# Kernel tuning notes

Measured on AMD Instinct MI355X. Metric: run time of the kernel, lower is better.

The kernel has to match this reference:

```python
import jax, jax.numpy as jnp
import numpy as np

N_NODES = 100000
IN_CH = 2
HID = 64
K = 3
N_EDGES = 1600000


def _cheb_norm(edge_index, num_nodes):
    # PyG ChebConv sym normalization with lambda_max=2.0:
    # L_hat = L - I = -D^{-1/2} A D^{-1/2} (zero diagonal, edge_weight=1)
    src, dst = edge_index[0], edge_index[1]
    deg = jax.ops.segment_sum(jnp.ones(src.shape[0], jnp.float32), src,
                              num_segments=num_nodes)
    dinv = jnp.where(deg > 0, jax.lax.rsqrt(jnp.maximum(deg, 1.0)), 0.0)
    norm = -dinv[src] * dinv[dst]  # [E]
    return src, dst, norm


def _cheb_conv(x, src, dst, norm, W, b, num_nodes):
    # W: [K, in, out], b: [out]
    def prop(t):  # sparse L_hat @ t via gather/scatter
        return jax.ops.segment_sum(norm[:, None] * t[src], dst,
                                   num_segments=num_nodes)
    Tx0 = x
    out = Tx0 @ W[0]
    Tx1 = prop(Tx0)
    out = out + Tx1 @ W[1]
    for k in range(2, W.shape[0]):
        Tx2 = 2.0 * prop(Tx1) - Tx0
        out = out + Tx2 @ W[k]
        Tx0, Tx1 = Tx1, Tx2
    return out + b


def setup_inputs() -> dict:
    key = jax.random.key(0)
    ks = jax.random.split(key, 16)
    x = jax.random.normal(ks[0], (N_NODES, IN_CH), jnp.float32)
    edge_index = jax.random.randint(ks[1], (2, N_EDGES), 0, N_NODES,
                                    dtype=jnp.int64)
    h = jax.random.normal(ks[2], (N_NODES, HID), jnp.float32)
    s1 = 1.0 / np.sqrt(IN_CH)
    s2 = 1.0 / np.sqrt(HID)
    sg = 1.0 / np.sqrt(2 * HID)
    W1 = jax.random.uniform(ks[3], (K, IN_CH, HID), jnp.float32, -s1, s1)
    b1 = jnp.zeros((HID,), jnp.float32)
    W2 = jax.random.uniform(ks[4], (K, HID, HID), jnp.float32, -s2, s2)
    b2 = jnp.zeros((HID,), jnp.float32)
    Wz = jax.random.uniform(ks[5], (2 * HID, HID), jnp.float32, -sg, sg)
    bz = jax.random.uniform(ks[6], (HID,), jnp.float32, -sg, sg)
    Wr = jax.random.uniform(ks[7], (2 * HID, HID), jnp.float32, -sg, sg)
    br = jax.random.uniform(ks[8], (HID,), jnp.float32, -sg, sg)
    Wc = jax.random.uniform(ks[9], (2 * HID, HID), jnp.float32, -sg, sg)
    bc = jax.random.uniform(ks[10], (HID,), jnp.float32, -sg, sg)
    return {"x": x, "edge_index": edge_index, "h": h,
            "W1": W1, "b1": b1, "W2": W2, "b2": b2,
            "Wz": Wz, "bz": bz, "Wr": Wr, "br": br, "Wc": Wc, "bc": bc}


def reference(x, edge_index, h, W1, b1, W2, b2, Wz, bz, Wr, br, Wc, bc):
    num_nodes = x.shape[0]
    src, dst, norm = _cheb_norm(edge_index, num_nodes)
    input_conv = _cheb_conv(x, src, dst, norm, W1, b1, num_nodes)
    hidden_conv = _cheb_conv(h, src, dst, norm, W2, b2, num_nodes)
    combined = jnp.concatenate([input_conv, hidden_conv], axis=1)
    z = jax.nn.sigmoid(combined @ Wz + bz)
    r = jax.nn.sigmoid(combined @ Wr + br)
    comb_c = jnp.concatenate([input_conv, r * hidden_conv], axis=1)
    h_tilde = jnp.tanh(comb_c @ Wc + bc)
    return z * h + (1.0 - z) * h_tilde
```

## Files before the change

### kernel.cpp

```cpp
#include <hip/hip_runtime.h>
#include <hip/hip_bf16.h>
#include <math.h>

#define HID 64
#define NBA 512
#define NBUCK 256
#define BSHIFT 9
#define BINS 512
#define NBN (NBUCK * NBA)

typedef __attribute__((ext_vector_type(8))) short bf16x8;
typedef __attribute__((ext_vector_type(4))) float f32x4;

__device__ __forceinline__ unsigned int bf16r(float f) {
    unsigned int u = __float_as_uint(f);
    return (u + 0x7fffu + ((u >> 16) & 1u)) >> 16;
}
__device__ __forceinline__ unsigned int pack2(float a, float b) {
    return bf16r(a) | (bf16r(b) << 16);
}
__device__ __forceinline__ float lo2f(unsigned int u) { return __uint_as_float(u << 16); }
__device__ __forceinline__ float hi2f(unsigned int u) { return __uint_as_float(u & 0xffff0000u); }

__device__ __forceinline__ bf16x8 asbf(uint4 u) {
    union { uint4 u4; bf16x8 b; } c; c.u4 = u; return c.b;
}
__device__ __forceinline__ void load8(const float* p, float* d) {
    float4 a = *(const float4*)p, b = *(const float4*)(p + 4);
    d[0]=a.x; d[1]=a.y; d[2]=a.z; d[3]=a.w; d[4]=b.x; d[5]=b.y; d[6]=b.z; d[7]=b.w;
}

__global__ void bucketA_kernel(const int* __restrict__ ei, int E,
                               int* __restrict__ cntsc) {
    __shared__ int cd[NBUCK], cs[NBUCK];
    int t = threadIdx.x;
    cd[t] = 0; cs[t] = 0;
    __syncthreads();
    int ce = (E + NBA - 1) / NBA;
    int e0 = blockIdx.x * ce, e1 = min(e0 + ce, E);
    for (int e = e0 + t; e < e1; e += 256) {
        int s = ei[e], d = ei[E + e];
        atomicAdd(&cs[s >> BSHIFT], 1);
        atomicAdd(&cd[d >> BSHIFT], 1);
    }
    __syncthreads();
    cntsc[t * NBA + blockIdx.x]       = cd[t];
    cntsc[NBN + t * NBA + blockIdx.x] = cs[t];
}

__global__ void scanA_kernel(const int* __restrict__ cnt, int* __restrict__ bs, int N) {
    __shared__ int s[256];
    int t = threadIdx.x, n = blockIdx.x * 256 + t;
    s[t] = (n < N) ? cnt[n] : 0;
    __syncthreads();
    for (int off = 128; off > 0; off >>= 1) {
        if (t < off) s[t] += s[t + off];
        __syncthreads();
    }
    if (t == 0) bs[blockIdx.x] = s[0];
}

__global__ void scanB_kernel(int* __restrict__ bs, int nb) {
    __shared__ int s[1024];
    int t = threadIdx.x;
    int orig = (t < nb) ? bs[t] : 0;
    s[t] = orig;
    __syncthreads();
    for (int off = 1; off < 1024; off <<= 1) {
        int v = (t >= off) ? s[t - off] : 0;
        __syncthreads();
        s[t] += v;
        __syncthreads();
    }
    if (t < nb) bs[t] = s[t] - orig;
}

__global__ void scanC_kernel(const int* __restrict__ cnt, const int* __restrict__ bs,
                             int* __restrict__ outp, int N) {
    __shared__ int s[256];
    int t = threadIdx.x, n = blockIdx.x * 256 + t;
    int c = (n < N) ? cnt[n] : 0;
    s[t] = c;
    __syncthreads();
    for (int off = 1; off < 256; off <<= 1) {
        int v = (t >= off) ? s[t - off] : 0;
        __syncthreads();
        s[t] += v;
        __syncthreads();
    }
    if (n < N) outp[n] = bs[blockIdx.x] + s[t] - c;
}

__global__ void bucketB_kernel(const int* __restrict__ ei, int E,
                               const int* __restrict__ scanned,
                               unsigned int* __restrict__ dstrec,
                               int* __restrict__ srckeys) {
    __shared__ int cd[NBUCK], cs[NBUCK], bd[NBUCK], bsr[NBUCK];
    int t = threadIdx.x;
    cd[t] = 0; cs[t] = 0;
    bd[t]  = scanned[t * NBA + blockIdx.x];
    bsr[t] = scanned[NBN + t * NBA + blockIdx.x] - E;
    __syncthreads();
    int ce = (E + NBA - 1) / NBA;
    int e0 = blockIdx.x * ce, e1 = min(e0 + ce, E);
    for (int e = e0 + t; e < e1; e += 256) {
        int s = ei[e], d = ei[E + e];
        int db = d >> BSHIFT, sb = s >> BSHIFT;
        int rd = atomicAdd(&cd[db], 1);
        dstrec[bd[db] + rd] = (unsigned int)s | ((unsigned int)(d & (BINS - 1)) << 17);
        int rs = atomicAdd(&cs[sb], 1);
        srckeys[bsr[sb] + rs] = s;
    }
}

__global__ void bucketC2_kernel(const int* __restrict__ srckeys,
                                const int* __restrict__ scanned,
                                float* __restrict__ dinv, int N, int E) {
    __shared__ int deg[BINS];
    int b = blockIdx.x, t = threadIdx.x;
    deg[t] = 0;
    __syncthreads();
    int start = scanned[NBN + b * NBA] - E;
    int end   = (b < NBUCK - 1) ? scanned[NBN + (b + 1) * NBA] - E : E;
    for (int i = start + t; i < end; i += BINS)
        atomicAdd(&deg[srckeys[i] & (BINS - 1)], 1);
    __syncthreads();
    int node = (b << BSHIFT) + t;
    if (node < N) {
        int dg = deg[t];
        dinv[node] = dg > 0 ? rsqrtf((float)dg) : 0.0f;
    }
}

__global__ void bucketC1_kernel(const unsigned int* __restrict__ dstrec,
                                const int* __restrict__ scanned,
                                const float* __restrict__ dinv,
                                int* __restrict__ row, int* __restrict__ cnt,
                                int2* __restrict__ srcw, int N, int E) {
    __shared__ int lc[BINS], ls[BINS], lr[BINS];
    int b = blockIdx.x, t = threadIdx.x;
    lc[t] = 0; lr[t] = 0;
    __syncthreads();
    int start = scanned[b * NBA];
    int end   = (b < NBUCK - 1) ? scanned[(b + 1) * NBA] : E;
    for (int i = start + t; i < end; i += BINS)
        atomicAdd(&lc[dstrec[i] >> 17], 1);
    __syncthreads();
    ls[t] = lc[t];
    __syncthreads();
    for (int off = 1; off < BINS; off <<= 1) {
        int v = (t >= off) ? ls[t - off] : 0;
        __syncthreads();
        ls[t] += v;
        __syncthreads();
    }
    int rl = start + ls[t] - lc[t];
    int node = (b << BSHIFT) + t;
    if (node < N) { row[node] = rl; cnt[node] = lc[t]; }
    __syncthreads();
    ls[t] = rl;
    __syncthreads();
    for (int i = start + t; i < end; i += BINS) {
        unsigned int rec = dstrec[i];
        int bin = (int)(rec >> 17);
        int src = (int)(rec & 0x1FFFFu);
        int p = ls[bin] + atomicAdd(&lr[bin], 1);
        srcw[p] = make_int2(src, __float_as_int(dinv[src]));
    }
}

__global__ void packwT_kernel(const float* __restrict__ W2, const float* __restrict__ Wz,
                              const float* __restrict__ Wr, const float* __restrict__ Wc,
                              unsigned int* __restrict__ WT) {
    int idx = blockIdx.x * blockDim.x + threadIdx.x;
    if (idx >= 18432) return;
    float v0, v1;
    if (idx < 6144) {
        int c = idx / 96, kk = idx % 96;
        int k0 = 2 * kk;
        if (k0 < 64) {
            v0 = W2[k0 * 64 + c] - W2[8192 + k0 * 64 + c];
            v1 = W2[(k0 + 1) * 64 + c] - W2[8192 + (k0 + 1) * 64 + c];
        } else if (k0 < 128) {
            v0 = W2[4096 + (k0 - 64) * 64 + c];
            v1 = W2[4096 + (k0 - 63) * 64 + c];
        } else {
            v0 = 2.0f * W2[8192 + (k0 - 128) * 64 + c];
            v1 = 2.0f * W2[8192 + (k0 - 127) * 64 + c];
        }
    } else if (idx < 14336) {
        int t = idx - 6144;
        int c = t / 64, kk = t % 64, k0 = 2 * kk;
        const float* Ws = (c < 64) ? Wz : Wr;
        int cc = c & 63;
        v0 = Ws[k0 * 64 + cc];
        v1 = Ws[(k0 + 1) * 64 + cc];
    } else {
        int t = idx - 14336;
        int c = t / 64, kk = t % 64, k0 = 2 * kk;
        v0 = Wc[k0 * 64 + c];
        v1 = Wc[(k0 + 1) * 64 + c];
    }
    WT[idx] = pack2(v0, v1);
}

__global__ void packh_kernel(const float* __restrict__ h, unsigned int* __restrict__ hbf,
                             int total2) {
    int i = blockIdx.x * blockDim.x + threadIdx.x;
    if (i < total2) {
        float2 v = ((const float2*)h)[i];
        hbf[i] = pack2(v.x, v.y);
    }
}

#define FMA8(ww, vv, xvv) \
    a0 = fmaf(ww, lo2f(vv.x), a0); a1 = fmaf(ww, hi2f(vv.x), a1); \
    a2 = fmaf(ww, lo2f(vv.y), a2); a3 = fmaf(ww, hi2f(vv.y), a3); \
    a4 = fmaf(ww, lo2f(vv.z), a4); a5 = fmaf(ww, hi2f(vv.z), a5); \
    a6 = fmaf(ww, lo2f(vv.w), a6); a7 = fmaf(ww, hi2f(vv.w), a7); \
    ax0 = fmaf(ww, xvv.x, ax0);    ax1 = fmaf(ww, xvv.y, ax1);

__global__ void gather64_kernel(const int* __restrict__ row, const int* __restrict__ cnt,
                                const int2* __restrict__ srcw, const float* __restrict__ dinv,
                                const unsigned int* __restrict__ src,
                                const float2* __restrict__ xsrc,
                                unsigned int* __restrict__ dst,
                                float2* __restrict__ xdst, int N) {
    int wu = __builtin_amdgcn_readfirstlane((int)threadIdx.x >> 6);
    int n = blockIdx.x * 4 + wu;
    if (n >= N) return;
    int lane = threadIdx.x & 63;
    int t    = lane & 7;
    int slot = lane >> 3;
    int start = row[n], k = cnt[n];
    float a0 = 0, a1 = 0, a2 = 0, a3 = 0, a4 = 0, a5 = 0, a6 = 0, a7 = 0;
    float ax0 = 0, ax1 = 0;
    if (k <= 16) {
        if (slot < k) {
            int2 rec0 = srcw[start + slot];
            bool h1 = slot + 8 < k;
            int2 rec1 = h1 ? srcw[start + slot + 8] : rec0;
            uint4 v0 = ((const uint4*)(src + (size_t)rec0.x * 32))[t];
            uint4 v1 = ((const uint4*)(src + (size_t)rec1.x * 32))[t];
            float2 xv0 = xsrc[rec0.x];
            float2 xv1 = xsrc[rec1.x];
            float w0 = __int_as_float(rec0.y);
            float w1 = h1 ? __int_as_float(rec1.y) : 0.0f;
            FMA8(w0, v0, xv0)
            FMA8(w1, v1, xv1)
        }
    } else {
        for (int e = slot; e < k; e += 32) {
            int2 rec0 = srcw[start + e];
            bool h1 = (e + 8) < k, h2 = (e + 16) < k, h3 = (e + 24) < k;
            int2 rec1 = h1 ? srcw[start + e + 8]  : rec0;
            int2 rec2 = h2 ? srcw[start + e + 16] : rec0;
            int2 rec3 = h3 ? srcw[start + e + 24] : rec0;
            uint4 v0 = ((const uint4*)(src + (size_t)rec0.x * 32))[t];
            uint4 v1 = ((const uint4*)(src + (size_t)rec1.x * 32))[t];
            uint4 v2 = ((const uint4*)(src + (size_t)rec2.x * 32))[t];
            uint4 v3 = ((const uint4*)(src + (size_t)rec3.x * 32))[t];
            float2 xv0 = xsrc[rec0.x];
            float2 xv1 = xsrc[rec1.x];
            float2 xv2 = xsrc[rec2.x];
            float2 xv3 = xsrc[rec3.x];
            float w0 = __int_as_float(rec0.y);
            float w1 = h1 ? __int_as_float(rec1.y) : 0.0f;
            float w2 = h2 ? __int_as_float(rec2.y) : 0.0f;
            float w3 = h3 ? __int_as_float(rec3.y) : 0.0f;
            FMA8(w0, v0, xv0)
            FMA8(w1, v1, xv1)
            FMA8(w2, v2, xv2)
            FMA8(w3, v3, xv3)
        }
    }
    a0 += __shfl_xor(a0, 8);  a1 += __shfl_xor(a1, 8);
    a2 += __shfl_xor(a2, 8);  a3 += __shfl_xor(a3, 8);
    a4 += __shfl_xor(a4, 8);  a5 += __shfl_xor(a5, 8);
    a6 += __shfl_xor(a6, 8);  a7 += __shfl_xor(a7, 8);
    ax0 += __shfl_xor(ax0, 8);  ax1 += __shfl_xor(ax1, 8);
    a0 += __shfl_xor(a0, 16); a1 += __shfl_xor(a1, 16);
    a2 += __shfl_xor(a2, 16); a3 += __shfl_xor(a3, 16);
    a4 += __shfl_xor(a4, 16); a5 += __shfl_xor(a5, 16);
    a6 += __shfl_xor(a6, 16); a7 += __shfl_xor(a7, 16);
    ax0 += __shfl_xor(ax0, 16); ax1 += __shfl_xor(ax1, 16);
    a0 += __shfl_xor(a0, 32); a1 += __shfl_xor(a1, 32);
    a2 += __shfl_xor(a2, 32); a3 += __shfl_xor(a3, 32);
    a4 += __shfl_xor(a4, 32); a5 += __shfl_xor(a5, 32);
    a6 += __shfl_xor(a6, 32); a7 += __shfl_xor(a7, 32);
    ax0 += __shfl_xor(ax0, 32); ax1 += __shfl_xor(ax1, 32);
    if (slot == 0) {
        float dn = -dinv[n];
        unsigned int* drow = dst + (size_t)n * 32;
        uint4 o;
        o.x = pack2(dn * a0, dn * a1);
        o.y = pack2(dn * a2, dn * a3);
        o.z = pack2(dn * a4, dn * a5);
        o.w = pack2(dn * a6, dn * a7);
        ((uint4*)drow)[t] = o;
        if (t == 0)
            xdst[n] = make_float2(dn * ax0, dn * ax1);
    }
}

__global__ __launch_bounds__(256, 2) void gate_mfma_kernel(
    float* __restrict__ out,
    const float* __restrict__ x,
    const float* __restrict__ h,
    const float* __restrict__ txa,
    const float* __restrict__ txb,
    const unsigned int* __restrict__ t1u,
    const unsigned int* __restrict__ ppu,
    const float* __restrict__ W1, const float* __restrict__ b1,
    const unsigned int* __restrict__ WT,
    const float* __restrict__ b2, const float* __restrict__ bz,
    const float* __restrict__ br, const float* __restrict__ bc,
    int N) {
    __shared__ __align__(16) unsigned int s_wzr[128 * 68];
    __shared__ __align__(16) unsigned int s_wc [64 * 68];
    __shared__ unsigned short tr[4][32][72];

    int tid  = threadIdx.x;
    int lane = tid & 63;
    int wu   = __builtin_amdgcn_readfirstlane(tid >> 6);
    int q    = lane >> 4;
    int r16  = lane & 15;
    int base = blockIdx.x * 128 + wu * 32;

    int nA[2];
    nA[0] = min(base + r16, N - 1);
    nA[1] = min(base + 16 + r16, N - 1);

    const unsigned int* W2eT = WT;

    {
        const uint4* wzr4 = (const uint4*)(WT + 6144);
        const uint4* wc4  = (const uint4*)(WT + 14336);
        #pragma unroll
        for (int i = 0; i < 8; ++i) {
            int idx4 = tid + i * 256;
            uint4 v = wzr4[idx4];
            int r = idx4 >> 4, c4 = (idx4 & 15) * 4;
            *(uint4*)&s_wzr[r * 68 + c4] = v;
        }
        #pragma unroll
        for (int i = 0; i < 4; ++i) {
            int idx4 = tid + i * 256;
            uint4 v = wc4[idx4];
            int r = idx4 >> 4, c4 = (idx4 & 15) * 4;
            *(uint4*)&s_wc[r * 68 + c4] = v;
        }
    }

    uint4 icA[2][2];
    {
        float2 xv[2], tav[2], tbv[2];
        #pragma unroll
        for (int mt = 0; mt < 2; ++mt) {
            xv[mt]  = ((const float2*)x)[nA[mt]];
            tav[mt] = ((const float2*)txa)[nA[mt]];
            tbv[mt] = ((const float2*)txb)[nA[mt]];
        }
        #pragma unroll
        for (int kf = 0; kf < 2; ++kf) {
            int ch0 = kf * 32 + 8 * q;
            float b1s[8], w0[8], w1s[8], w2[8], w3[8], w4[8], w5[8];
            load8(b1 + ch0, b1s);
            load8(W1 + ch0, w0);       load8(W1 + 64 + ch0, w1s);
            load8(W1 + 128 + ch0, w2); load8(W1 + 192 + ch0, w3);
            load8(W1 + 256 + ch0, w4); load8(W1 + 320 + ch0, w5);
            #pragma unroll
            for (int mt = 0; mt < 2; ++mt) {
                float t20 = 2.0f * tbv[mt].x - xv[mt].x;
                float t21 = 2.0f * tbv[mt].y - xv[mt].y;
                unsigned int pr[4];
                #pragma unroll
                for (int p = 0; p < 4; ++p) {
                    float v0 = b1s[2*p]   + xv[mt].x * w0[2*p]   + xv[mt].y * w1s[2*p]
                             + tav[mt].x * w2[2*p]   + tav[mt].y * w3[2*p]
                             + t20 * w4[2*p]   + t21 * w5[2*p];
                    float v1 = b1s[2*p+1] + xv[mt].x * w0[2*p+1] + xv[mt].y * w1s[2*p+1]
                             + tav[mt].x * w2[2*p+1] + tav[mt].y * w3[2*p+1]
                             + t20 * w4[2*p+1] + t21 * w5[2*p+1];
                    pr[p] = pack2(v0, v1);
                }
                icA[mt][kf] = make_uint4(pr[0], pr[1], pr[2], pr[3]);
            }
        }
    }

    f32x4 acc1[2][4];
    #pragma unroll
    for (int mt = 0; mt < 2; ++mt)
        #pragma unroll
        for (int nt = 0; nt < 4; ++nt)
            acc1[mt][nt] = (f32x4){0.0f, 0.0f, 0.0f, 0.0f};

    #pragma unroll
    for (int ks = 0; ks < 6; ++ks) {
        bf16x8 a[2];
        if (ks < 2) {
            #pragma unroll
            for (int mt = 0; mt < 2; ++mt) {
                float hs[8];
                load8(h + (size_t)nA[mt] * 64 + ks * 32 + 8 * q, hs);
                uint4 u;
                u.x = pack2(hs[0], hs[1]); u.y = pack2(hs[2], hs[3]);
                u.z = pack2(hs[4], hs[5]); u.w = pack2(hs[6], hs[7]);
                a[mt] = asbf(u);
            }
        } else {
            const unsigned int* tab = (ks < 4) ? t1u : ppu;
            int ksl = ks & 1;
            #pragma unroll
            for (int mt = 0; mt < 2; ++mt)
                a[mt] = asbf(*(const uint4*)(tab + (size_t)nA[mt] * 32 + ksl * 16 + q * 4));
        }
        #pragma unroll
        for (int nt = 0; nt < 4; ++nt) {
            bf16x8 b = asbf(*(const uint4*)(W2eT + (nt * 16 + r16) * 96 + ks * 16 + q * 4));
            #pragma unroll
            for (int mt = 0; mt < 2; ++mt)
                acc1[mt][nt] = __builtin_amdgcn_mfma_f32_16x16x32_bf16(a[mt], b, acc1[mt][nt], 0, 0, 0);
        }
    }

    __syncthreads();

    float b2v[4];
    #pragma unroll
    for (int nt = 0; nt < 4; ++nt) b2v[nt] = b2[nt * 16 + r16];
    #pragma unroll
    for (int mt = 0; mt < 2; ++mt)
        #pragma unroll
        for (int nt = 0; nt < 4; ++nt)
            #pragma unroll
            for (int reg = 0; reg < 4; ++reg) {
                acc1[mt][nt][reg] += b2v[nt];
                tr[wu][mt * 16 + 4 * q + reg][nt * 16 + r16] =
                    (unsigned short)bf16r(acc1[mt][nt][reg]);
            }
    __builtin_amdgcn_wave_barrier();
    bf16x8 hcA[2][2];
    #pragma unroll
    for (int mt = 0; mt < 2; ++mt)
        #pragma unroll
        for (int kf = 0; kf < 2; ++kf)
            hcA[mt][kf] = asbf(*(const uint4*)&tr[wu][mt * 16 + r16][kf * 32 + 8 * q]);
    __builtin_amdgcn_wave_barrier();

    f32x4 acc2[2][8];
    #pragma unroll
    for (int mt = 0; mt < 2; ++mt)
        #pragma unroll
        for (int nt = 0; nt < 8; ++nt)
            acc2[mt][nt] = (f32x4){0.0f, 0.0f, 0.0f, 0.0f};

    #pragma unroll
    for (int kf = 0; kf < 4; ++kf) {
        bf16x8 a[2];
        a[0] = (kf < 2) ? asbf(icA[0][kf]) : hcA[0][kf - 2];
        a[1] = (kf < 2) ? asbf(icA[1][kf]) : hcA[1][kf - 2];
        #pragma unroll
        for (int nt = 0; nt < 8; ++nt) {
            bf16x8 b = asbf(*(const uint4*)&s_wzr[(nt * 16 + r16) * 68 + kf * 16 + q * 4]);
            #pragma unroll
            for (int mt = 0; mt < 2; ++mt)
                acc2[mt][nt] = __builtin_amdgcn_mfma_f32_16x16x32_bf16(a[mt], b, acc2[mt][nt], 0, 0, 0);
        }
    }

    float bzv[4], brv[4];
    #pragma unroll
    for (int nt = 0; nt < 4; ++nt) { bzv[nt] = bz[nt * 16 + r16]; brv[nt] = br[nt * 16 + r16]; }
    float zz[2][4][4];
    #pragma unroll
    for (int mt = 0; mt < 2; ++mt)
        #pragma unroll
        for (int nt = 0; nt < 4; ++nt)
            #pragma unroll
            for (int reg = 0; reg < 4; ++reg) {
                zz[mt][nt][reg] = 1.0f / (1.0f + __expf(-(acc2[mt][nt][reg] + bzv[nt])));
                float rr = 1.0f / (1.0f + __expf(-(acc2[mt][nt + 4][reg] + brv[nt])));
                float rhc = rr * acc1[mt][nt][reg];
                tr[wu][mt * 16 + 4 * q + reg][nt * 16 + r16] = (unsigned short)bf16r(rhc);
            }
    __builtin_amdgcn_wave_barrier();
    bf16x8 rhcA[2][2];
    #pragma unroll
    for (int mt = 0; mt < 2; ++mt)
        #pragma unroll
        for (int kf = 0; kf < 2; ++kf)
            rhcA[mt][kf] = asbf(*(const uint4*)&tr[wu][mt * 16 + r16][kf * 32 + 8 * q]);
    __builtin_amdgcn_wave_barrier();

    f32x4 acc3[2][4];
    #pragma unroll
    for (int mt = 0; mt < 2; ++mt)
        #pragma unroll
        for (int nt = 0; nt < 4; ++nt)
            acc3[mt][nt] = (f32x4){0.0f, 0.0f, 0.0f, 0.0f};

    #pragma unroll
    for (int kf = 0; kf < 4; ++kf) {
        bf16x8 a[2];
        a[0] = (kf < 2) ? asbf(icA[0][kf]) : rhcA[0][kf - 2];
        a[1] = (kf < 2) ? asbf(icA[1][kf]) : rhcA[1][kf - 2];
        #pragma unroll
        for (int nt = 0; nt < 4; ++nt) {
            bf16x8 b = asbf(*(const uint4*)&s_wc[(nt * 16 + r16) * 68 + kf * 16 + q * 4]);
            #pragma unroll
            for (int mt = 0; mt < 2; ++mt)
                acc3[mt][nt] = __builtin_amdgcn_mfma_f32_16x16x32_bf16(a[mt], b, acc3[mt][nt], 0, 0, 0);
        }
    }

    float bcv[4];
    #pragma unroll
    for (int nt = 0; nt < 4; ++nt) bcv[nt] = bc[nt * 16 + r16];
    #pragma unroll
    for (int mt = 0; mt < 2; ++mt)
        #pragma unroll
        for (int nt = 0; nt < 4; ++nt)
            #pragma unroll
            for (int reg = 0; reg < 4; ++reg) {
                int node = base + mt * 16 + 4 * q + reg;
                if (node < N) {
                    float a = acc3[mt][nt][reg] + bcv[nt];
                    a = fminf(fmaxf(a, -40.0f), 40.0f);
                    float e = __expf(2.0f * a);
                    float ht = 1.0f - 2.0f / (e + 1.0f);
                    float hv = h[(size_t)node * 64 + nt * 16 + r16];
                    float z = zz[mt][nt][reg];
                    out[(size_t)node * 64 + nt * 16 + r16] = z * hv + (1.0f - z) * ht;
                }
            }
}

extern "C" void kernel_launch(void* const* d_in, const int* in_sizes, int n_in,
                              void* d_out, int out_size, void* d_ws, size_t ws_size,
                              hipStream_t stream) {
    const float* x  = (const float*)d_in[0];
    const int*   ei = (const int*)  d_in[1];
    const float* h  = (const float*)d_in[2];
    const float* W1 = (const float*)d_in[3];
    const float* b1 = (const float*)d_in[4];
    const float* W2 = (const float*)d_in[5];
    const float* b2 = (const float*)d_in[6];
    const float* Wz = (const float*)d_in[7];
    const float* bz = (const float*)d_in[8];
    const float* Wr = (const float*)d_in[9];
    const float* br = (const float*)d_in[10];
    const float* Wc = (const float*)d_in[11];
    const float* bc = (const float*)d_in[12];
    float* out = (float*)d_out;

    int N = in_sizes[0] / 2;
    int E = in_sizes[1] / 2;

    char* wsb = (char*)d_ws;
    float* dinv = (float*)wsb;
    int*   row  = (int*)  (wsb + (size_t)N * 4);
    int*   cnt  = (int*)  (wsb + (size_t)2 * N * 4);
    float* txa  = (float*)(wsb + (size_t)3 * N * 4);
    float* txb  = (float*)(wsb + (size_t)5 * N * 4);
    int*   bs   = (int*)  (wsb + (size_t)7 * N * 4);
    unsigned int* WT = (unsigned int*)(wsb + ((size_t)7 * N + 1024) * 4);
    int*   cntsc   = (int*)(wsb + ((size_t)7 * N + 19456) * 4);
    int*   scanned = (int*)(wsb + ((size_t)7 * N + 19456 + 2 * NBN) * 4);
    int2*  srcw = (int2*)(wsb + ((size_t)7 * N + 19456 + 4 * NBN) * 4);
    size_t O = (size_t)7 * N + 19456 + 4 * (size_t)NBN + 2 * (size_t)E;
    unsigned int* bufA = (unsigned int*)(wsb + O * 4);
    unsigned int* hpp  = (unsigned int*)(wsb + (O + (size_t)32 * N) * 4);
    unsigned int* dstrec = (unsigned int*)(wsb + O * 4);
    int* srckeys = (int*)(wsb + (O + (size_t)E) * 4);

    bucketA_kernel<<<NBA, 256, 0, stream>>>(ei, E, cntsc);
    int scn = 2 * NBN;
    scanA_kernel<<<scn / 256, 256, 0, stream>>>(cntsc, bs, scn);
    scanB_kernel<<<1, 1024, 0, stream>>>(bs, scn / 256);
    scanC_kernel<<<scn / 256, 256, 0, stream>>>(cntsc, bs, scanned, scn);
    bucketB_kernel<<<NBA, 256, 0, stream>>>(ei, E, scanned, dstrec, srckeys);
    bucketC2_kernel<<<NBUCK, BINS, 0, stream>>>(srckeys, scanned, dinv, N, E);
    bucketC1_kernel<<<NBUCK, BINS, 0, stream>>>(dstrec, scanned, dinv, row, cnt, srcw, N, E);

    packwT_kernel<<<(18432 + 255) / 256, 256, 0, stream>>>(W2, Wz, Wr, Wc, WT);
    packh_kernel <<<(32 * N + 255) / 256, 256, 0, stream>>>(h, hpp, 32 * N);

    int gblocks = (N + 3) / 4;
    gather64_kernel<<<gblocks, 256, 0, stream>>>(row, cnt, srcw, dinv, hpp,
                                                 (const float2*)x, bufA,
                                                 (float2*)txa, N);
    gather64_kernel<<<gblocks, 256, 0, stream>>>(row, cnt, srcw, dinv, bufA,
                                                 (const float2*)txa, hpp,
                                                 (float2*)txb, N);

    int gateblocks = (N + 127) / 128;
    gate_mfma_kernel<<<gateblocks, 256, 0, stream>>>(
        out, x, h, txa, txb, bufA, hpp, W1, b1, WT, b2, bz, br, bc, N);
}
```

Baseline: 215.9 us.

## Store CSR sources as u32, gather dinv on the fly, reuse bf16 h in gate

The CSR edge records shrink from an (src, dinv) int2 pair to a single 32-bit source index, and the gather kernels now look up dinv[src] directly. This cuts edge-list write and read traffic in half at the cost of an extra random (likely cached) load per edge. The gate kernel now reads the bf16-packed copy of h instead of fp32 h, both for the MFMA input and for the final blend. That halves h traffic but uses bf16-rounded h in the z*h output term, which reduces precision. Workspace layout is adjusted to keep hbf separate from the hpp buffer that the second gather overwrites.

```diff
diff --git a/kernel.cpp b/kernel.cpp
--- a/kernel.cpp
+++ b/kernel.cpp
@@ -134,9 +134,8 @@
 
 __global__ void bucketC1_kernel(const unsigned int* __restrict__ dstrec,
                                 const int* __restrict__ scanned,
-                                const float* __restrict__ dinv,
                                 int* __restrict__ row, int* __restrict__ cnt,
-                                int2* __restrict__ srcw, int N, int E) {
+                                unsigned int* __restrict__ srcu, int N, int E) {
     __shared__ int lc[BINS], ls[BINS], lr[BINS];
     int b = blockIdx.x, t = threadIdx.x;
     lc[t] = 0; lr[t] = 0;
@@ -163,9 +162,8 @@
     for (int i = start + t; i < end; i += BINS) {
         unsigned int rec = dstrec[i];
         int bin = (int)(rec >> 17);
-        int src = (int)(rec & 0x1FFFFu);
         int p = ls[bin] + atomicAdd(&lr[bin], 1);
-        srcw[p] = make_int2(src, __float_as_int(dinv[src]));
+        srcu[p] = rec & 0x1FFFFu;
     }
 }
 
@@ -221,7 +219,8 @@
     ax0 = fmaf(ww, xvv.x, ax0);    ax1 = fmaf(ww, xvv.y, ax1);
 
 __global__ void gather64_kernel(const int* __restrict__ row, const int* __restrict__ cnt,
-                                const int2* __restrict__ srcw, const float* __restrict__ dinv,
+                                const unsigned int* __restrict__ srcu,
+                                const float* __restrict__ dinv,
                                 const unsigned int* __restrict__ src,
                                 const float2* __restrict__ xsrc,
                                 unsigned int* __restrict__ dst,
@@ -237,37 +236,37 @@
     float ax0 = 0, ax1 = 0;
     if (k <= 16) {
         if (slot < k) {
-            int2 rec0 = srcw[start + slot];
+            unsigned int s0 = srcu[start + slot];
             bool h1 = slot + 8 < k;
-            int2 rec1 = h1 ? srcw[start + slot + 8] : rec0;
-            uint4 v0 = ((const uint4*)(src + (size_t)rec0.x * 32))[t];
-            uint4 v1 = ((const uint4*)(src + (size_t)rec1.x * 32))[t];
-            float2 xv0 = xsrc[rec0.x];
-            float2 xv1 = xsrc[rec1.x];
-            float w0 = __int_as_float(rec0.y);
-            float w1 = h1 ? __int_as_float(rec1.y) : 0.0f;
+            unsigned int s1 = h1 ? srcu[start + slot + 8] : s0;
+            uint4 v0 = ((const uint4*)(src + (size_t)s0 * 32))[t];
+            uint4 v1 = ((const uint4*)(src + (size_t)s1 * 32))[t];
+            float2 xv0 = xsrc[s0];
+            float2 xv1 = xsrc[s1];
+            float w0 = dinv[s0];
+            float w1 = h1 ? dinv[s1] : 0.0f;
             FMA8(w0, v0, xv0)
             FMA8(w1, v1, xv1)
         }
     } else {
         for (int e = slot; e < k; e += 32) {
-            int2 rec0 = srcw[start + e];
+            unsigned int s0 = srcu[start + e];
             bool h1 = (e + 8) < k, h2 = (e + 16) < k, h3 = (e + 24) < k;
-            int2 rec1 = h1 ? srcw[start + e + 8]  : rec0;
-            int2 rec2 = h2 ? srcw[start + e + 16] : rec0;
-            int2 rec3 = h3 ? srcw[start + e + 24] : rec0;
-            uint4 v0 = ((const uint4*)(src + (size_t)rec0.x * 32))[t];
-            uint4 v1 = ((const uint4*)(src + (size_t)rec1.x * 32))[t];
-            uint4 v2 = ((const uint4*)(src + (size_t)rec2.x * 32))[t];
-            uint4 v3 = ((const uint4*)(src + (size_t)rec3.x * 32))[t];
-            float2 xv0 = xsrc[rec0.x];
-            float2 xv1 = xsrc[rec1.x];
-            float2 xv2 = xsrc[rec2.x];
-            float2 xv3 = xsrc[rec3.x];
-            float w0 = __int_as_float(rec0.y);
-            float w1 = h1 ? __int_as_float(rec1.y) : 0.0f;
-            float w2 = h2 ? __int_as_float(rec2.y) : 0.0f;
-            float w3 = h3 ? __int_as_float(rec3.y) : 0.0f;
+            unsigned int s1 = h1 ? srcu[start + e + 8]  : s0;
+            unsigned int s2 = h2 ? srcu[start + e + 16] : s0;
+            unsigned int s3 = h3 ? srcu[start + e + 24] : s0;
+            uint4 v0 = ((const uint4*)(src + (size_t)s0 * 32))[t];
+            uint4 v1 = ((const uint4*)(src + (size_t)s1 * 32))[t];
+            uint4 v2 = ((const uint4*)(src + (size_t)s2 * 32))[t];
+            uint4 v3 = ((const uint4*)(src + (size_t)s3 * 32))[t];
+            float2 xv0 = xsrc[s0];
+            float2 xv1 = xsrc[s1];
+            float2 xv2 = xsrc[s2];
+            float2 xv3 = xsrc[s3];
+            float w0 = dinv[s0];
+            float w1 = h1 ? dinv[s1] : 0.0f;
+            float w2 = h2 ? dinv[s2] : 0.0f;
+            float w3 = h3 ? dinv[s3] : 0.0f;
             FMA8(w0, v0, xv0)
             FMA8(w1, v1, xv1)
             FMA8(w2, v2, xv2)
@@ -306,7 +305,7 @@
 __global__ __launch_bounds__(256, 2) void gate_mfma_kernel(
     float* __restrict__ out,
     const float* __restrict__ x,
-    const float* __restrict__ h,
+    const unsigned int* __restrict__ hbf,
     const float* __restrict__ txa,
     const float* __restrict__ txb,
     const unsigned int* __restrict__ t1u,
@@ -398,24 +397,12 @@
 
     #pragma unroll
     for (int ks = 0; ks < 6; ++ks) {
+        const unsigned int* tab = (ks < 2) ? hbf : ((ks < 4) ? t1u : ppu);
+        int ksl = ks & 1;
         bf16x8 a[2];
-        if (ks < 2) {
-            #pragma unroll
-            for (int mt = 0; mt < 2; ++mt) {
-                float hs[8];
-                load8(h + (size_t)nA[mt] * 64 + ks * 32 + 8 * q, hs);
-                uint4 u;
-                u.x = pack2(hs[0], hs[1]); u.y = pack2(hs[2], hs[3]);
-                u.z = pack2(hs[4], hs[5]); u.w = pack2(hs[6], hs[7]);
-                a[mt] = asbf(u);
-            }
-        } else {
-            const unsigned int* tab = (ks < 4) ? t1u : ppu;
-            int ksl = ks & 1;
-            #pragma unroll
-            for (int mt = 0; mt < 2; ++mt)
-                a[mt] = asbf(*(const uint4*)(tab + (size_t)nA[mt] * 32 + ksl * 16 + q * 4));
-        }
+        #pragma unroll
+        for (int mt = 0; mt < 2; ++mt)
+            a[mt] = asbf(*(const uint4*)(tab + (size_t)nA[mt] * 32 + ksl * 16 + q * 4));
         #pragma unroll
         for (int nt = 0; nt < 4; ++nt) {
             bf16x8 b = asbf(*(const uint4*)(W2eT + (nt * 16 + r16) * 96 + ks * 16 + q * 4));
@@ -530,7 +517,8 @@
                     a = fminf(fmaxf(a, -40.0f), 40.0f);
                     float e = __expf(2.0f * a);
                     float ht = 1.0f - 2.0f / (e + 1.0f);
-                    float hv = h[(size_t)node * 64 + nt * 16 + r16];
+                    unsigned int hu = hbf[(size_t)node * 32 + nt * 8 + (r16 >> 1)];
+                    float hv = (r16 & 1) ? hi2f(hu) : lo2f(hu);
                     float z = zz[mt][nt][reg];
                     out[(size_t)node * 64 + nt * 16 + r16] = z * hv + (1.0f - z) * ht;
                 }
@@ -568,10 +556,11 @@
     unsigned int* WT = (unsigned int*)(wsb + ((size_t)7 * N + 1024) * 4);
     int*   cntsc   = (int*)(wsb + ((size_t)7 * N + 19456) * 4);
     int*   scanned = (int*)(wsb + ((size_t)7 * N + 19456 + 2 * NBN) * 4);
-    int2*  srcw = (int2*)(wsb + ((size_t)7 * N + 19456 + 4 * NBN) * 4);
-    size_t O = (size_t)7 * N + 19456 + 4 * (size_t)NBN + 2 * (size_t)E;
-    unsigned int* bufA = (unsigned int*)(wsb + O * 4);
-    unsigned int* hpp  = (unsigned int*)(wsb + (O + (size_t)32 * N) * 4);
+    unsigned int* srcu = (unsigned int*)(wsb + ((size_t)7 * N + 19456 + 4 * NBN) * 4);
+    size_t O = (size_t)7 * N + 19456 + 4 * (size_t)NBN + (size_t)E;
+    unsigned int* hbf  = (unsigned int*)(wsb + O * 4);
+    unsigned int* bufA = (unsigned int*)(wsb + (O + (size_t)32 * N) * 4);
+    unsigned int* hpp  = (unsigned int*)(wsb + (O + (size_t)64 * N) * 4);
     unsigned int* dstrec = (unsigned int*)(wsb + O * 4);
     int* srckeys = (int*)(wsb + (O + (size_t)E) * 4);
 
@@ -582,20 +571,20 @@
     scanC_kernel<<<scn / 256, 256, 0, stream>>>(cntsc, bs, scanned, scn);
     bucketB_kernel<<<NBA, 256, 0, stream>>>(ei, E, scanned, dstrec, srckeys);
     bucketC2_kernel<<<NBUCK, BINS, 0, stream>>>(srckeys, scanned, dinv, N, E);
-    bucketC1_kernel<<<NBUCK, BINS, 0, stream>>>(dstrec, scanned, dinv, row, cnt, srcw, N, E);
+    bucketC1_kernel<<<NBUCK, BINS, 0, stream>>>(dstrec, scanned, row, cnt, srcu, N, E);
 
     packwT_kernel<<<(18432 + 255) / 256, 256, 0, stream>>>(W2, Wz, Wr, Wc, WT);
-    packh_kernel <<<(32 * N + 255) / 256, 256, 0, stream>>>(h, hpp, 32 * N);
+    packh_kernel <<<(32 * N + 255) / 256, 256, 0, stream>>>(h, hbf, 32 * N);
 
     int gblocks = (N + 3) / 4;
-    gather64_kernel<<<gblocks, 256, 0, stream>>>(row, cnt, srcw, dinv, hpp,
+    gather64_kernel<<<gblocks, 256, 0, stream>>>(row, cnt, srcu, dinv, hbf,
                                                  (const float2*)x, bufA,
                                                  (float2*)txa, N);
-    gather64_kernel<<<gblocks, 256, 0, stream>>>(row, cnt, srcw, dinv, bufA,
+    gather64_kernel<<<gblocks, 256, 0, stream>>>(row, cnt, srcu, dinv, bufA,
                                                  (const float2*)txa, hpp,
                                                  (float2*)txb, N);
 
     int gateblocks = (N + 127) / 128;
     gate_mfma_kernel<<<gateblocks, 256, 0, stream>>>(
-        out, x, h, txa, txb, bufA, hpp, W1, b1, WT, b2, bz, br, bc, N);
-}
+        out, x, hbf, txa, txb, bufA, hpp, W1, b1, WT, b2, bz, br, bc, N);
+}
```

New measurement: 204.1 us, median of 2. 5.4% less time.
